# Optimization experiments

Hardware: AMD Instinct MI355X
Metric: run time of the kernel (lower is better)

Reference implementation:

```python
import jax, jax.numpy as jnp
import numpy as np

T, C, H, W = 16, 3, 512, 512
PS, PT = 7, 1
NQ = 262144


def setup_inputs() -> dict:
    key = jax.random.key(0)
    k1, k2, k3, k4 = jax.random.split(key, 4)
    vid2fill = jnp.zeros((T, C, H, W), jnp.float32)
    patches = jax.random.normal(k1, (NQ, PT, C, PS, PS), jnp.float32)
    # queryInds columns: (t, h, w) top-left corners, each kept in-bounds
    qt = jax.random.randint(k2, (NQ, 1), 0, T - PT + 1)
    qh = jax.random.randint(k3, (NQ, 1), 0, H - PS + 1)
    qw = jax.random.randint(k4, (NQ, 1), 0, W - PS + 1)
    queryInds = jnp.concatenate([qt, qh, qw], axis=1).astype(jnp.int32)
    return {"vid2fill": vid2fill, "patches": patches, "queryInds": queryInds}


def reference(vid2fill, patches, queryInds):
    # vid2fill: [T,C,H,W]; patches: [N,pt,C,ps,ps]; queryInds: [N,3] = (t,h,w)
    T_, C_, H_, W_ = vid2fill.shape
    N, pt, _, ps, _ = patches.shape
    ti = queryInds[:, 0, None] + jnp.arange(pt)  # [N,pt]
    hi = queryInds[:, 1, None] + jnp.arange(ps)  # [N,ps]
    wi = queryInds[:, 2, None] + jnp.arange(ps)  # [N,ps]
    # flat spatial-temporal index over (t,h,w): [N,pt,ps,ps]
    flat = (ti[:, :, None, None] * H_ + hi[:, None, :, None]) * W_ + wi[:, None, None, :]
    # channels-last flat video [T*H*W, C] for a single vectorized scatter-add
    vid_flat = vid2fill.transpose(0, 2, 3, 1).reshape(-1, C_)
    p = patches.transpose(0, 1, 3, 4, 2).reshape(-1, C_)  # [N*pt*ps*ps, C]
    out = vid_flat.at[flat.reshape(-1)].add(p)
    return out.reshape(T_, H_, W_, C_).transpose(0, 3, 1, 2)
```

## Files before the change

kernel.cpp:

```cpp
#include <hip/hip_runtime.h>

constexpr int T_ = 16, C_ = 3, H_ = 512, W_ = 512, PS_ = 7;
constexpr int PATCH_ELEMS = C_ * PS_ * PS_;
constexpr int TILE  = 32;
constexpr int HALO  = PS_ - 1;
constexpr int LTILE = TILE + HALO;
constexpr int NTH = H_ / TILE, NTW = W_ / TILE;
constexpr int NBINS = T_ * NTH * NTW;
constexpr int LDS_PER_C  = LTILE * LTILE;
constexpr int ACC_FLOATS = C_ * LDS_PER_C;
constexpr int INTERIOR   = C_ * TILE * TILE;
constexpr int HALO_A = HALO * LTILE;
constexpr int HALO_B = TILE * HALO;
constexpr int HALO_PER_C    = HALO_A + HALO_B;
constexpr int HALO_PER_TILE = C_ * HALO_PER_C;
constexpr int CAP = 160;
constexpr int BTHR = 192;

constexpr size_t OFF_COUNTS = 0;
constexpr size_t OFF_LIST   = 16384;
constexpr size_t OFF_HALO   = OFF_LIST + (size_t)NBINS * CAP * 4;
constexpr size_t WS_NEEDED  = OFF_HALO + (size_t)NBINS * HALO_PER_TILE * 4;

__global__ void zero_counts_kernel(int* counts) {
    counts[blockIdx.x * 1024 + threadIdx.x] = 0;
}

__global__ void scatter_kernel(const int* __restrict__ q, int* __restrict__ counts,
                               int* __restrict__ list, int nq) {
    int n = blockIdx.x * 256 + threadIdx.x;
    if (n >= nq) return;
    int t = q[3 * n], h = q[3 * n + 1], w = q[3 * n + 2];
    int bin = (t * NTH + (h >> 5)) * NTW + (w >> 5);
    int pos = atomicAdd(counts + bin, 1);
    if (pos < CAP) list[bin * CAP + pos] = (n << 10) | ((h & 31) << 5) | (w & 31);
}

__global__ __launch_bounds__(BTHR, 4) void accum_kernel(
    const float* __restrict__ patches, const int* __restrict__ counts,
    const int* __restrict__ list, const float* __restrict__ vid,
    float* __restrict__ out, float* __restrict__ halo) {
    __shared__ float acc[ACC_FLOATS];
    __shared__ int recs[CAP];
    const int bin = blockIdx.x;
    const int t = bin >> 8;
    const int h0 = ((bin >> 4) & 15) * TILE, w0 = (bin & 15) * TILE;
    const int tid = threadIdx.x;
    const int lane = tid & 63, wid = tid >> 6;

    for (int k = tid; k < ACC_FLOATS; k += BTHR) acc[k] = 0.f;
    int cnt = counts[bin];
    if (cnt > CAP) cnt = CAP;
    if (tid < cnt) recs[tid] = list[bin * CAP + tid];
    __syncthreads();

    {
        const bool act = lane < PS_ * PS_;
        const int loff = act ? (lane / PS_) * LTILE + (lane % PS_) : 0;
        float* __restrict__ ac = acc + wid * LDS_PER_C;
        const float* __restrict__ pc = patches + wid * (PS_ * PS_);

        float v0=0.f,v1=0.f,v2=0.f,v3=0.f,v4=0.f,v5=0.f,v6=0.f,v7=0.f;
        int b0=0,b1=0,b2=0,b3=0,b4=0,b5=0,b6=0,b7=0;
#define LDR(vv,bb,ii) { int rr = recs[(ii)]; \
                        bb = ((rr >> 5) & 31) * LTILE + (rr & 31); \
                        vv = act ? pc[(size_t)(rr >> 10) * PATCH_ELEMS + lane] : 0.f; }
        if (0 < cnt) LDR(v0,b0,0)
        if (1 < cnt) LDR(v1,b1,1)
        if (2 < cnt) LDR(v2,b2,2)
        if (3 < cnt) LDR(v3,b3,3)
        if (4 < cnt) LDR(v4,b4,4)
        if (5 < cnt) LDR(v5,b5,5)
        if (6 < cnt) LDR(v6,b6,6)
        if (7 < cnt) LDR(v7,b7,7)
        for (int p = 0; p < cnt; p += 8) {
            float u0=v0,u1=v1,u2=v2,u3=v3,u4=v4,u5=v5,u6=v6,u7=v7;
            int c0=b0,c1=b1,c2=b2,c3=b3,c4=b4,c5=b5,c6=b6,c7=b7;
            int q = p + 8;
            if (q     < cnt) LDR(v0,b0,q)
            if (q + 1 < cnt) LDR(v1,b1,q+1)
            if (q + 2 < cnt) LDR(v2,b2,q+2)
            if (q + 3 < cnt) LDR(v3,b3,q+3)
            if (q + 4 < cnt) LDR(v4,b4,q+4)
            if (q + 5 < cnt) LDR(v5,b5,q+5)
            if (q + 6 < cnt) LDR(v6,b6,q+6)
            if (q + 7 < cnt) LDR(v7,b7,q+7)
            if (act) {
                ac[c0 + loff] += u0;
                if (p + 1 < cnt) ac[c1 + loff] += u1;
                if (p + 2 < cnt) ac[c2 + loff] += u2;
                if (p + 3 < cnt) ac[c3 + loff] += u3;
                if (p + 4 < cnt) ac[c4 + loff] += u4;
                if (p + 5 < cnt) ac[c5 + loff] += u5;
                if (p + 6 < cnt) ac[c6 + loff] += u6;
                if (p + 7 < cnt) ac[c7 + loff] += u7;
            }
        }
#undef LDR
    }
    __syncthreads();

    const size_t obase = (size_t)t * C_ * H_ * W_;
    for (int k = tid; k < INTERIOR; k += BTHR) {
        int c = k >> 10, rem = k & 1023, y = rem >> 5, x = rem & 31;
        size_t g = obase + (size_t)c * (H_ * W_) + (size_t)(h0 + y) * W_ + (w0 + x);
        out[g] = vid[g] + acc[c * LDS_PER_C + y * LTILE + x];
    }
    float* hp = halo + (size_t)bin * HALO_PER_TILE;
    for (int k = tid; k < HALO_PER_TILE; k += BTHR) {
        int c = k / HALO_PER_C, r = k % HALO_PER_C;
        int y, x;
        if (r < HALO_A) { y = TILE + r / LTILE; x = r % LTILE; }
        else            { int r2 = r - HALO_A; y = r2 / HALO; x = TILE + r2 % HALO; }
        hp[k] = acc[c * LDS_PER_C + y * LTILE + x];
    }
}

__global__ void halo_add_kernel(const float* __restrict__ halo,
                                float* __restrict__ out, int total) {
    int idx = blockIdx.x * 256 + threadIdx.x;
    if (idx >= total) return;
    int w = idx & (W_ - 1);
    int h = (idx >> 9) & (H_ - 1);
    int ct = idx >> 18;
    int c = ct % C_, t = ct / C_;
    int hm = h & (TILE - 1), wm = w & (TILE - 1);
    bool top  = (hm < HALO) && (h >= TILE);
    bool left = (wm < HALO) && (w >= TILE);
    if (!(top || left)) return;
    int i = h >> 5, j = w >> 5;
    float a = 0.f;
    if (top) {
        int tb = (t * NTH + (i - 1)) * NTW + j;
        a += halo[(size_t)tb * HALO_PER_TILE + c * HALO_PER_C + hm * LTILE + wm];
    }
    if (left) {
        int tb = (t * NTH + i) * NTW + (j - 1);
        a += halo[(size_t)tb * HALO_PER_TILE + c * HALO_PER_C + HALO_A + hm * HALO + wm];
    }
    if (top && left) {
        int tb = (t * NTH + (i - 1)) * NTW + (j - 1);
        a += halo[(size_t)tb * HALO_PER_TILE + c * HALO_PER_C + hm * LTILE + (TILE + wm)];
    }
    out[idx] += a;
}

__global__ void scatter_add_kernel(const float* __restrict__ patches,
                                   const int* __restrict__ qinds,
                                   float* __restrict__ out, int total) {
    int tid = blockIdx.x * blockDim.x + threadIdx.x;
    if (tid >= total) return;
    int n = tid / PATCH_ELEMS;
    int r = tid - n * PATCH_ELEMS;
    int c = r / (PS_ * PS_);
    int rr = r - c * (PS_ * PS_);
    int ih = rr / PS_, iw = rr - ih * PS_;
    int t = qinds[n * 3 + 0], h = qinds[n * 3 + 1], w = qinds[n * 3 + 2];
    int out_idx = ((t * C_ + c) * H_ + (h + ih)) * W_ + (w + iw);
    atomicAdd(out + out_idx, patches[tid]);
}

extern "C" void kernel_launch(void* const* d_in, const int* in_sizes, int n_in,
                              void* d_out, int out_size, void* d_ws, size_t ws_size,
                              hipStream_t stream) {
    const float* vid     = (const float*)d_in[0];
    const float* patches = (const float*)d_in[1];
    const int*   qinds   = (const int*)d_in[2];
    float*       out     = (float*)d_out;
    const int nq = in_sizes[2] / 3;

    if (ws_size < WS_NEEDED) {
        hipMemcpyAsync(out, vid, (size_t)out_size * sizeof(float),
                       hipMemcpyDeviceToDevice, stream);
        int total = nq * PATCH_ELEMS;
        scatter_add_kernel<<<(total + 255) / 256, 256, 0, stream>>>(patches, qinds, out, total);
        return;
    }

    char* ws = (char*)d_ws;
    int*   counts = (int*)(ws + OFF_COUNTS);
    int*   list   = (int*)(ws + OFF_LIST);
    float* halo   = (float*)(ws + OFF_HALO);

    zero_counts_kernel<<<NBINS / 1024, 1024, 0, stream>>>(counts);
    scatter_kernel<<<(nq + 255) / 256, 256, 0, stream>>>(qinds, counts, list, nq);
    accum_kernel<<<NBINS, BTHR, 0, stream>>>(patches, counts, list, vid, out, halo);
    int total = T_ * C_ * H_ * W_;
    halo_add_kernel<<<(total + 255) / 256, 256, 0, stream>>>(halo, out, total);
}
```

Measured before the change: 339.3 us.

## Split per-tile patch list across two wave groups and launch halo add only on bands

Doubles the accumulation block to 384 threads. Each channel's patch list is split between two waves, and each wave accumulates into its own LDS plane, so the 2x-larger LDS accumulators are summed at writeback. The LDS row stride is padded to 40 so the interior writeback can use float4 vid loads and out stores. The halo add kernel now launches only over the halo band pixels of each tile instead of the whole video. The cost is more LDS per block, which may lower occupancy.

Result: faster. 325.3 us (-4.1%).

```diff
diff --git a/kernel.cpp b/kernel.cpp
--- a/kernel.cpp
+++ b/kernel.cpp
@@ -5,17 +5,20 @@
 constexpr int TILE  = 32;
 constexpr int HALO  = PS_ - 1;
 constexpr int LTILE = TILE + HALO;
+constexpr int LSTRIDE = 40;
 constexpr int NTH = H_ / TILE, NTW = W_ / TILE;
 constexpr int NBINS = T_ * NTH * NTW;
-constexpr int LDS_PER_C  = LTILE * LTILE;
-constexpr int ACC_FLOATS = C_ * LDS_PER_C;
+constexpr int LDS_PER_C  = LTILE * LSTRIDE;
+constexpr int NPLANES = 6;
+constexpr int ACC_FLOATS = NPLANES * LDS_PER_C;
 constexpr int INTERIOR   = C_ * TILE * TILE;
 constexpr int HALO_A = HALO * LTILE;
 constexpr int HALO_B = TILE * HALO;
 constexpr int HALO_PER_C    = HALO_A + HALO_B;
 constexpr int HALO_PER_TILE = C_ * HALO_PER_C;
 constexpr int CAP = 160;
-constexpr int BTHR = 192;
+constexpr int BTHR = 384;
+constexpr int BAND = HALO * TILE + (TILE - HALO) * HALO;
 
 constexpr size_t OFF_COUNTS = 0;
 constexpr size_t OFF_LIST   = 16384;
@@ -36,7 +39,7 @@
     if (pos < CAP) list[bin * CAP + pos] = (n << 10) | ((h & 31) << 5) | (w & 31);
 }
 
-__global__ __launch_bounds__(BTHR, 4) void accum_kernel(
+__global__ __launch_bounds__(BTHR, 6) void accum_kernel(
     const float* __restrict__ patches, const int* __restrict__ counts,
     const int* __restrict__ list, const float* __restrict__ vid,
     float* __restrict__ out, float* __restrict__ halo) {
@@ -47,8 +50,9 @@
     const int h0 = ((bin >> 4) & 15) * TILE, w0 = (bin & 15) * TILE;
     const int tid = threadIdx.x;
     const int lane = tid & 63, wid = tid >> 6;
-
-    for (int k = tid; k < ACC_FLOATS; k += BTHR) acc[k] = 0.f;
+    const int c = wid >> 1, k = wid & 1;
+
+    for (int i = tid; i < ACC_FLOATS; i += BTHR) acc[i] = 0.f;
     int cnt = counts[bin];
     if (cnt > CAP) cnt = CAP;
     if (tid < cnt) recs[tid] = list[bin * CAP + tid];
@@ -56,44 +60,46 @@
 
     {
         const bool act = lane < PS_ * PS_;
-        const int loff = act ? (lane / PS_) * LTILE + (lane % PS_) : 0;
-        float* __restrict__ ac = acc + wid * LDS_PER_C;
-        const float* __restrict__ pc = patches + wid * (PS_ * PS_);
-
-        float v0=0.f,v1=0.f,v2=0.f,v3=0.f,v4=0.f,v5=0.f,v6=0.f,v7=0.f;
-        int b0=0,b1=0,b2=0,b3=0,b4=0,b5=0,b6=0,b7=0;
-#define LDR(vv,bb,ii) { int rr = recs[(ii)]; \
-                        bb = ((rr >> 5) & 31) * LTILE + (rr & 31); \
-                        vv = act ? pc[(size_t)(rr >> 10) * PATCH_ELEMS + lane] : 0.f; }
-        if (0 < cnt) LDR(v0,b0,0)
-        if (1 < cnt) LDR(v1,b1,1)
-        if (2 < cnt) LDR(v2,b2,2)
-        if (3 < cnt) LDR(v3,b3,3)
-        if (4 < cnt) LDR(v4,b4,4)
-        if (5 < cnt) LDR(v5,b5,5)
-        if (6 < cnt) LDR(v6,b6,6)
-        if (7 < cnt) LDR(v7,b7,7)
-        for (int p = 0; p < cnt; p += 8) {
-            float u0=v0,u1=v1,u2=v2,u3=v3,u4=v4,u5=v5,u6=v6,u7=v7;
-            int c0=b0,c1=b1,c2=b2,c3=b3,c4=b4,c5=b5,c6=b6,c7=b7;
-            int q = p + 8;
-            if (q     < cnt) LDR(v0,b0,q)
-            if (q + 1 < cnt) LDR(v1,b1,q+1)
-            if (q + 2 < cnt) LDR(v2,b2,q+2)
-            if (q + 3 < cnt) LDR(v3,b3,q+3)
-            if (q + 4 < cnt) LDR(v4,b4,q+4)
-            if (q + 5 < cnt) LDR(v5,b5,q+5)
-            if (q + 6 < cnt) LDR(v6,b6,q+6)
-            if (q + 7 < cnt) LDR(v7,b7,q+7)
+        const int loff = act ? (lane / PS_) * LSTRIDE + (lane % PS_) : 0;
+        float* __restrict__ ac = acc + (k * 3 + c) * LDS_PER_C;
+        const float* __restrict__ pc = patches + c * (PS_ * PS_);
+        const int lo = (k * cnt) >> 1;
+        const int hi = ((k + 1) * cnt) >> 1;
+
+        float v0=0,v1=0,v2=0,v3=0,v4=0,v5=0,v6=0,v7=0;
+        int o0=0,o1=0,o2=0,o3=0,o4=0,o5=0,o6=0,o7=0;
+#define LDR(vv,oo,ii) { int rr = recs[(ii)]; \
+        oo = ((rr >> 5) & 31) * LSTRIDE + (rr & 31) + loff; \
+        vv = act ? pc[(unsigned)(rr >> 10) * (unsigned)PATCH_ELEMS + lane] : 0.f; }
+        if (lo     < hi) LDR(v0,o0, lo)
+        if (lo + 1 < hi) LDR(v1,o1, lo+1)
+        if (lo + 2 < hi) LDR(v2,o2, lo+2)
+        if (lo + 3 < hi) LDR(v3,o3, lo+3)
+        if (lo + 4 < hi) LDR(v4,o4, lo+4)
+        if (lo + 5 < hi) LDR(v5,o5, lo+5)
+        if (lo + 6 < hi) LDR(v6,o6, lo+6)
+        if (lo + 7 < hi) LDR(v7,o7, lo+7)
+        for (int p = lo; p < hi; p += 8) {
+            float x0=v0,x1=v1,x2=v2,x3=v3,x4=v4,x5=v5,x6=v6,x7=v7;
+            int q0=o0,q1=o1,q2=o2,q3=o3,q4=o4,q5=o5,q6=o6,q7=o7;
+            int qq = p + 8;
+            if (qq     < hi) LDR(v0,o0, qq)
+            if (qq + 1 < hi) LDR(v1,o1, qq+1)
+            if (qq + 2 < hi) LDR(v2,o2, qq+2)
+            if (qq + 3 < hi) LDR(v3,o3, qq+3)
+            if (qq + 4 < hi) LDR(v4,o4, qq+4)
+            if (qq + 5 < hi) LDR(v5,o5, qq+5)
+            if (qq + 6 < hi) LDR(v6,o6, qq+6)
+            if (qq + 7 < hi) LDR(v7,o7, qq+7)
             if (act) {
-                ac[c0 + loff] += u0;
-                if (p + 1 < cnt) ac[c1 + loff] += u1;
-                if (p + 2 < cnt) ac[c2 + loff] += u2;
-                if (p + 3 < cnt) ac[c3 + loff] += u3;
-                if (p + 4 < cnt) ac[c4 + loff] += u4;
-                if (p + 5 < cnt) ac[c5 + loff] += u5;
-                if (p + 6 < cnt) ac[c6 + loff] += u6;
-                if (p + 7 < cnt) ac[c7 + loff] += u7;
+                ac[q0] += x0;
+                if (p + 1 < hi) ac[q1] += x1;
+                if (p + 2 < hi) ac[q2] += x2;
+                if (p + 3 < hi) ac[q3] += x3;
+                if (p + 4 < hi) ac[q4] += x4;
+                if (p + 5 < hi) ac[q5] += x5;
+                if (p + 6 < hi) ac[q6] += x6;
+                if (p + 7 < hi) ac[q7] += x7;
             }
         }
 #undef LDR
@@ -101,18 +107,26 @@
     __syncthreads();
 
     const size_t obase = (size_t)t * C_ * H_ * W_;
-    for (int k = tid; k < INTERIOR; k += BTHR) {
-        int c = k >> 10, rem = k & 1023, y = rem >> 5, x = rem & 31;
-        size_t g = obase + (size_t)c * (H_ * W_) + (size_t)(h0 + y) * W_ + (w0 + x);
-        out[g] = vid[g] + acc[c * LDS_PER_C + y * LTILE + x];
+    for (int i = tid; i < INTERIOR / 4; i += BTHR) {
+        int cc = i >> 8, rem = i & 255, y = rem >> 3, x4 = rem & 7;
+        size_t g = obase + (size_t)cc * (H_ * W_) + (size_t)(h0 + y) * W_ + (w0 + x4 * 4);
+        const float4 vv = *reinterpret_cast<const float4*>(vid + g);
+        const int ao = cc * LDS_PER_C + y * LSTRIDE + x4 * 4;
+        const float4 aa = *reinterpret_cast<const float4*>(&acc[ao]);
+        const float4 bb = *reinterpret_cast<const float4*>(&acc[ao + 3 * LDS_PER_C]);
+        float4 r;
+        r.x = vv.x + aa.x + bb.x; r.y = vv.y + aa.y + bb.y;
+        r.z = vv.z + aa.z + bb.z; r.w = vv.w + aa.w + bb.w;
+        *reinterpret_cast<float4*>(out + g) = r;
     }
     float* hp = halo + (size_t)bin * HALO_PER_TILE;
-    for (int k = tid; k < HALO_PER_TILE; k += BTHR) {
-        int c = k / HALO_PER_C, r = k % HALO_PER_C;
+    for (int i = tid; i < HALO_PER_TILE; i += BTHR) {
+        int cc = i / HALO_PER_C, r = i % HALO_PER_C;
         int y, x;
         if (r < HALO_A) { y = TILE + r / LTILE; x = r % LTILE; }
         else            { int r2 = r - HALO_A; y = r2 / HALO; x = TILE + r2 % HALO; }
-        hp[k] = acc[c * LDS_PER_C + y * LTILE + x];
+        int ao = cc * LDS_PER_C + y * LSTRIDE + x;
+        hp[i] = acc[ao] + acc[ao + 3 * LDS_PER_C];
     }
 }
 
@@ -120,15 +134,17 @@
                                 float* __restrict__ out, int total) {
     int idx = blockIdx.x * 256 + threadIdx.x;
     if (idx >= total) return;
-    int w = idx & (W_ - 1);
-    int h = (idx >> 9) & (H_ - 1);
-    int ct = idx >> 18;
-    int c = ct % C_, t = ct / C_;
-    int hm = h & (TILE - 1), wm = w & (TILE - 1);
-    bool top  = (hm < HALO) && (h >= TILE);
-    bool left = (wm < HALO) && (w >= TILE);
+    int bin = idx / (C_ * BAND);
+    int r = idx - bin * (C_ * BAND);
+    int c = r / BAND;
+    int s = r - c * BAND;
+    int hm, wm;
+    if (s < HALO * TILE) { hm = s >> 5; wm = s & 31; }
+    else { int s2 = s - HALO * TILE; hm = HALO + s2 / HALO; wm = s2 - (s2 / HALO) * HALO; }
+    int t = bin >> 8, i = (bin >> 4) & 15, j = bin & 15;
+    bool top  = (hm < HALO) && (i > 0);
+    bool left = (wm < HALO) && (j > 0);
     if (!(top || left)) return;
-    int i = h >> 5, j = w >> 5;
     float a = 0.f;
     if (top) {
         int tb = (t * NTH + (i - 1)) * NTW + j;
@@ -142,7 +158,8 @@
         int tb = (t * NTH + (i - 1)) * NTW + (j - 1);
         a += halo[(size_t)tb * HALO_PER_TILE + c * HALO_PER_C + hm * LTILE + (TILE + wm)];
     }
-    out[idx] += a;
+    size_t g = (((size_t)t * C_ + c) * H_ + (i * TILE + hm)) * W_ + (j * TILE + wm);
+    out[g] += a;
 }
 
 __global__ void scatter_add_kernel(const float* __restrict__ patches,
@@ -185,6 +202,6 @@
     zero_counts_kernel<<<NBINS / 1024, 1024, 0, stream>>>(counts);
     scatter_kernel<<<(nq + 255) / 256, 256, 0, stream>>>(qinds, counts, list, nq);
     accum_kernel<<<NBINS, BTHR, 0, stream>>>(patches, counts, list, vid, out, halo);
-    int total = T_ * C_ * H_ * W_;
-    halo_add_kernel<<<(total + 255) / 256, 256, 0, stream>>>(halo, out, total);
-}
+    int total_band = NBINS * C_ * BAND;
+    halo_add_kernel<<<(total_band + 255) / 256, 256, 0, stream>>>(halo, out, total_band);
+}
```
